# Kernel tuning notes

Hardware: AMD Instinct MI355X
Metric: run time of the kernel (lower is better)

The kernel has to match this reference:

```python
import jax, jax.numpy as jnp
import numpy as np

ST_HIDDEN = 128
ST_HEADS = 4
ST_LAYERS = 3
RES_SCALE = 1.0
DK = ST_HIDDEN // ST_HEADS


def build_3d_adj(spatial_ei, spatial_ea, n_nodes, window):
    # replicate spatial edges per time slice with node offset t*n_nodes
    offs = (jnp.arange(window) * n_nodes)[None, :, None]  # [1,W,1]
    all_sp_idx = (spatial_ei[:, None, :] + offs).reshape(2, -1)  # [2, W*E]
    all_sp_attr = jnp.tile(spatial_ea, (window, 1))  # [W*E, De]
    # temporal edges t -> t+1 for every node
    src = jnp.arange((window - 1) * n_nodes)
    temp_idx = jnp.stack([src, src + n_nodes], axis=0)  # [2, (W-1)*N]
    temp_attr = jnp.broadcast_to(spatial_ea.mean(axis=0, keepdims=True),
                                 (temp_idx.shape[1], spatial_ea.shape[1]))
    ei = jnp.concatenate([all_sp_idx, temp_idx], axis=1)
    ea = jnp.concatenate([all_sp_attr, temp_attr], axis=0)
    return ei, ea


def seg_softmax(logits, dst, num_nodes):
    # logits [E,H], segment softmax over dst (pyg_softmax)
    m = jax.ops.segment_max(logits, dst, num_segments=num_nodes)  # [N,H]
    ex = jnp.exp(logits - m[dst])
    s = jax.ops.segment_sum(ex, dst, num_segments=num_nodes)
    return ex / (s[dst] + 1e-16)


def layernorm(x, g, b, eps=1e-5):
    mu = x.mean(-1, keepdims=True)
    var = ((x - mu) ** 2).mean(-1, keepdims=True)
    return (x - mu) * jax.lax.rsqrt(var + eps) * g + b


def block(x, ei, ea, qw, qb, kw, kb, vw, vb, fw, fb, ow, ob, ln_g, ln_b):
    B, Nt, _ = x.shape
    H, dk = ST_HEADS, DK
    Q = (x @ qw + qb).reshape(B, Nt, H, dk)
    K = (x @ kw + kb).reshape(B, Nt, H, dk)
    V = (x @ vw + vb).reshape(B, Nt, H, dk)
    src, dst = ei[0], ei[1]
    q_e = Q[:, dst]  # [B,E,H,dk]
    k_e = K[:, src]
    v_e = V[:, src]
    film = ea @ fw + fb  # [E, 2*hidden]
    gamma, beta = jnp.split(film, 2, axis=-1)
    gamma = gamma.reshape(1, -1, H, dk)
    beta = beta.reshape(1, -1, H, dk)
    k_e = k_e * (1.0 + gamma) + beta
    logits = (q_e * k_e).sum(-1) / np.sqrt(dk).astype(np.float32)  # [B,E,H]
    att = jax.vmap(lambda l: seg_softmax(l, dst, Nt))(logits)
    msg = att[..., None] * v_e  # [B,E,H,dk]
    out = jnp.zeros((B, Nt, H, dk), x.dtype).at[:, dst].add(msg)
    y = out.reshape(B, Nt, H * dk) @ ow + ob
    return layernorm(x + y, ln_g, ln_b)


def setup_inputs() -> dict:
    key = jax.random.key(0)
    ks = jax.random.split(key, 12)
    B, W, N, Fin, E, De = 2, 16, 1000, 16, 16000, 8
    H, L = ST_HIDDEN, ST_LAYERS
    g = lambda k, s: jax.random.normal(k, s, jnp.float32) * 0.05
    return {
        "xw": jax.random.normal(ks[0], (B, W, N, Fin), jnp.float32),
        "spatial_ei": jax.random.randint(ks[1], (2, E), 0, N),
        "spatial_ea": jax.random.normal(ks[2], (E, De), jnp.float32),
        "in_w": g(ks[3], (Fin, H)), "in_b": jnp.zeros((H,), jnp.float32),
        "qw": g(ks[4], (L, H, H)), "qb": jnp.zeros((L, H), jnp.float32),
        "kw": g(ks[5], (L, H, H)), "kb": jnp.zeros((L, H), jnp.float32),
        "vw": g(ks[6], (L, H, H)), "vb": jnp.zeros((L, H), jnp.float32),
        "fw": g(ks[7], (L, De, 2 * H)), "fb": jnp.zeros((L, 2 * H), jnp.float32),
        "ow": g(ks[8], (L, H, H)), "ob": jnp.zeros((L, H), jnp.float32),
        "ln_g": jnp.ones((L, H), jnp.float32), "ln_b": jnp.zeros((L, H), jnp.float32),
        "head_w": g(ks[9], (H, 1)), "head_b": jnp.zeros((1,), jnp.float32),
    }


def reference(xw, spatial_ei, spatial_ea, in_w, in_b, qw, qb, kw, kb, vw, vb,
              fw, fb, ow, ob, ln_g, ln_b, head_w, head_b):
    B, W, N, Fin = xw.shape
    ei, ea = build_3d_adj(spatial_ei, spatial_ea, N, W)
    x = xw.reshape(B, W * N, Fin) @ in_w + in_b
    for l in range(ST_LAYERS):
        bx = block(x, ei, ea, qw[l], qb[l], kw[l], kb[l], vw[l], vb[l],
                   fw[l], fb[l], ow[l], ob[l], ln_g[l], ln_b[l])
        x = x + RES_SCALE * (bx - x)
    last = x.reshape(B, W, N, -1)[:, -1]  # [B,N,H]
    return jax.nn.softplus(last @ head_w + head_b).squeeze(-1)  # [B,N]
```

## Files before the change

kernel.cpp:

```cpp
#include <hip/hip_runtime.h>
#include <math.h>

constexpr int B    = 2;
constexpr int W    = 16;
constexpr int N    = 1000;
constexpr int FIN  = 16;
constexpr int E    = 16000;
constexpr int DE   = 8;
constexpr int H    = 128;
constexpr int L    = 3;
constexpr int WL   = 4;
constexpr int W0G  = 12;
constexpr int RPB  = WL * N;
constexpr int ROWS = B * RPB;
constexpr int NMAT = 12;

__device__ __forceinline__ float blockSum128(float v) {
  #pragma unroll
  for (int off = 32; off >= 1; off >>= 1) v += __shfl_xor(v, off);
  __shared__ float s2[2];
  int w = threadIdx.x >> 6;
  __syncthreads();
  if ((threadIdx.x & 63) == 0) s2[w] = v;
  __syncthreads();
  return s2[0] + s2[1];
}

__device__ __forceinline__ float dpp_add_xor1(float x) {
  int y = __builtin_amdgcn_update_dpp(0, __float_as_int(x), 0xB1, 0xF, 0xF, true);
  return x + __int_as_float(y);
}
__device__ __forceinline__ float dpp_add_xor2(float x) {
  int y = __builtin_amdgcn_update_dpp(0, __float_as_int(x), 0x4E, 0xF, 0xF, true);
  return x + __int_as_float(y);
}
__device__ __forceinline__ float headSum32(float p) {
  p = dpp_add_xor1(p);
  p = dpp_add_xor2(p);
  p += __shfl_xor(p, 4);
  p += __shfl_xor(p, 8);
  p += __shfl_xor(p, 16);
  return p;
}
__device__ __forceinline__ float dot4(float4 a, float4 b) {
  return a.x * b.x + a.y * b.y + a.z * b.z + a.w * b.w;
}

__global__ void k_count_scan(const int* __restrict__ ei, int* __restrict__ offs,
                             int* __restrict__ cursor, float* __restrict__ meanea) {
  __shared__ int cnt[N];
  __shared__ int scn[1024];
  int t = threadIdx.x;
  if (t < 8) meanea[t] = 0.f;
  if (t < N) cnt[t] = 0;
  __syncthreads();
  int vals[16];
  int nv = 0;
  for (int e = t; e < E; e += 1024) vals[nv++] = ei[E + e];
  for (int i = 0; i < nv; i++) atomicAdd(&cnt[vals[i]], 1);
  __syncthreads();
  int v = (t < N) ? cnt[t] : 0;
  scn[t] = v;
  __syncthreads();
  for (int st = 1; st < 1024; st <<= 1) {
    int add = (t >= st) ? scn[t - st] : 0;
    __syncthreads();
    scn[t] += add;
    __syncthreads();
  }
  if (t < N) {
    offs[t + 1] = scn[t];
    if (t == 0) offs[0] = 0;
    cursor[t] = scn[t] - v;
  }
}

__global__ void k_prep2(const int* __restrict__ ei, const float* __restrict__ ea,
                        int* __restrict__ cursor, int* __restrict__ csr_src,
                        int* __restrict__ csr_eid, float* __restrict__ meanea,
                        const float* __restrict__ qw, const float* __restrict__ kw,
                        const float* __restrict__ vw, const float* __restrict__ ow,
                        float4* __restrict__ wTp4,
                        const float* __restrict__ xw, const float* __restrict__ in_w,
                        const float* __restrict__ in_b, float* __restrict__ x) {
  int bid = blockIdx.x;
  int t = threadIdx.x;
  if (bid < 64) {
    int e = bid * 256 + t;
    if (e < E) {
      int src = ei[e];
      int dst = ei[E + e];
      int pos = atomicAdd(&cursor[dst], 1);
      csr_src[pos] = src;
      csr_eid[pos] = e;
    }
  } else if (bid < 128) {
    __shared__ float sbuf[256];
    int d = t & 7, g = t >> 3;
    float s = 0.f;
    for (int e = (bid - 64) * 32 + g; e < E; e += 64 * 32) s += ea[e * DE + d];
    sbuf[t] = s;
    __syncthreads();
    for (int st = 16; st >= 1; st >>= 1) {
      if (g < st) sbuf[g * 8 + d] += sbuf[(g + st) * 8 + d];
      __syncthreads();
    }
    if (g == 0) atomicAdd(&meanea[d], sbuf[d]);
  } else if (bid < 128 + NMAT * 16) {
    int bid2 = bid - 128;
    int mat = bid2 / 16;
    int pair = bid2 % 16;
    int kk4 = pair * 2 + (t >> 7);
    int c = t & 127;
    int l = mat >> 2, mm = mat & 3;
    const float* src = ((mm == 0) ? qw : (mm == 1) ? kw : (mm == 2) ? vw : ow) + (long)l * H * H;
    int k0 = kk4 * 4;
    float4 v4;
    v4.x = src[(k0 + 0) * H + c];
    v4.y = src[(k0 + 1) * H + c];
    v4.z = src[(k0 + 2) * H + c];
    v4.w = src[(k0 + 3) * H + c];
    wTp4[((long)mat * 32 + kk4) * H + c] = v4;
  } else {
    int bi = bid - (128 + NMAT * 16);
    int b = bi / 63, tt = bi % 63;
    int lr0 = tt * 64;
    __shared__ float xwS[64][FIN];
    __shared__ float inS[FIN][H];
    for (int i = t; i < 64 * FIN; i += 256) {
      int r = i >> 4, k = i & 15;
      int lr = lr0 + r;
      float val = 0.f;
      if (lr < RPB) {
        int wl = lr / N, n = lr % N;
        val = xw[(((long)b * W + (W0G + wl)) * N + n) * FIN + k];
      }
      xwS[r][k] = val;
    }
    for (int i = t; i < FIN * H; i += 256) inS[i >> 7][i & 127] = in_w[i];
    __syncthreads();
    #pragma unroll
    for (int qi = 0; qi < 8; qi++) {
      int idx = t + qi * 256;
      int r = idx >> 5, cq = idx & 31;
      int lr = lr0 + r;
      if (lr < RPB) {
        float4 acc = *(const float4*)(in_b + cq * 4);
        #pragma unroll
        for (int k = 0; k < FIN; k++) {
          float xv = xwS[r][k];
          float4 w4 = *(const float4*)(&inS[k][cq * 4]);
          acc.x += xv * w4.x; acc.y += xv * w4.y; acc.z += xv * w4.z; acc.w += xv * w4.w;
        }
        *(float4*)(x + ((long)b * RPB + lr) * H + cq * 4) = acc;
      }
    }
  }
}

__global__ void k_gemm(const float* __restrict__ X, const float4* __restrict__ wTp4,
                       int matBase,
                       const float* __restrict__ bq, const float* __restrict__ bk,
                       const float* __restrict__ bv,
                       float* __restrict__ Cq, float* __restrict__ Ck, float* __restrict__ Cv,
                       int base, int tiles) {
  int m = blockIdx.y;
  const float* bm = (m == 0) ? bq : (m == 1) ? bk : bv;
  float* Cm       = (m == 0) ? Cq : (m == 1) ? Ck : Cv;
  const float4* wp = wTp4 + (long)(matBase + m) * 32 * H;
  int bb = blockIdx.x / tiles;
  int tt = blockIdx.x % tiles;
  int lr0 = base + tt * 64;
  int t = threadIdx.x;
  int cg = t & 31, rg = t >> 5;
  __shared__ float xs[64][H];
  #pragma unroll
  for (int i = 0; i < 8; i++) {
    int row = i * 8 + rg;
    int lr = lr0 + row;
    float4 v4 = make_float4(0.f, 0.f, 0.f, 0.f);
    if (lr < RPB) v4 = *(const float4*)(X + ((long)bb * RPB + lr) * H + cg * 4);
    *(float4*)&xs[row][cg * 4] = v4;
  }
  __syncthreads();
  float4 bias4 = *(const float4*)(bm + cg * 4);
  float4 acc[8];
  #pragma unroll
  for (int i = 0; i < 8; i++) acc[i] = bias4;
  for (int kk4 = 0; kk4 < 32; kk4++) {
    float4 w0 = wp[kk4 * H + cg * 4 + 0];
    float4 w1 = wp[kk4 * H + cg * 4 + 1];
    float4 w2 = wp[kk4 * H + cg * 4 + 2];
    float4 w3 = wp[kk4 * H + cg * 4 + 3];
    #pragma unroll
    for (int i = 0; i < 8; i++) {
      float4 xv = *(const float4*)&xs[rg * 8 + i][kk4 * 4];
      acc[i].x += dot4(xv, w0);
      acc[i].y += dot4(xv, w1);
      acc[i].z += dot4(xv, w2);
      acc[i].w += dot4(xv, w3);
    }
  }
  #pragma unroll
  for (int i = 0; i < 8; i++) {
    int lr = lr0 + rg * 8 + i;
    if (lr < RPB) *(float4*)(Cm + ((long)bb * RPB + lr) * H + cg * 4) = acc[i];
  }
}

__global__ void k_attn_oln(const float* __restrict__ Qb, const float* __restrict__ Kb,
                           const float* __restrict__ Vb,
                           const float* __restrict__ ea, const float* __restrict__ meanea,
                           const float* __restrict__ fw, const float* __restrict__ fb,
                           const int* __restrict__ offs, const int* __restrict__ csr_src,
                           const int* __restrict__ csr_eid,
                           const float* __restrict__ x, const float4* __restrict__ owp,
                           const float* __restrict__ ob, const float* __restrict__ lng,
                           const float* __restrict__ lnb, float* __restrict__ xo,
                           int out_lo,
                           const float* __restrict__ hw, const float* __restrict__ hb,
                           float* __restrict__ out, int do_head) {
  int tid = threadIdx.x;
  float rgw[DE], rbw[DE];
  #pragma unroll
  for (int d = 0; d < DE; d++) {
    rgw[d] = fw[d * 2 * H + tid];
    rbw[d] = fw[d * 2 * H + H + tid];
  }
  int nwin = WL - out_lo;
  int idx = blockIdx.x;
  int b = idx / (nwin * N);
  int rem = idx % (nwin * N);
  int wl = out_lo + rem / N;
  int n = rem % N;
  long drow = ((long)b * WL + wl) * N + n;
  float q = Qb[drow * H + tid];
  float fbg = fb[tid], fbb = fb[H + tid];
  long sbase = ((long)b * WL + wl) * N;
  long trow  = ((long)b * WL + wl - 1) * N + n;
  const float scale = 0.17677669529663687f;
  int i0 = offs[n], i1 = offs[n + 1];

  float m = -INFINITY, ssum = 0.f, acc = 0.f;
  for (int base = i0; base <= i1; base += 4) {
    float l[4], vv[4];
    #pragma unroll
    for (int j = 0; j < 4; j++) {
      int i = base + j;
      if (i > i1) { l[j] = -INFINITY; vv[j] = 0.f; continue; }
      long srow; const float* eap; float esc;
      if (i < i1) { srow = sbase + csr_src[i]; eap = ea + (long)csr_eid[i] * DE; esc = 1.f; }
      else        { srow = trow;               eap = meanea;                    esc = 1.f / E; }
      float kv = Kb[srow * H + tid];
      vv[j]    = Vb[srow * H + tid];
      float4 a0 = *(const float4*)(eap);
      float4 a1 = *(const float4*)(eap + 4);
      float a[DE] = {a0.x * esc, a0.y * esc, a0.z * esc, a0.w * esc,
                     a1.x * esc, a1.y * esc, a1.z * esc, a1.w * esc};
      float g = fbg, be = fbb;
      #pragma unroll
      for (int d = 0; d < DE; d++) {
        g  += a[d] * rgw[d];
        be += a[d] * rbw[d];
      }
      float p = q * (kv * (1.f + g) + be);
      l[j] = headSum32(p) * scale;
    }
    float mn = m;
    #pragma unroll
    for (int j = 0; j < 4; j++) mn = fmaxf(mn, l[j]);
    float sc  = __expf(m - mn);
    float pe0 = __expf(l[0] - mn);
    float pe1 = __expf(l[1] - mn);
    float pe2 = __expf(l[2] - mn);
    float pe3 = __expf(l[3] - mn);
    ssum = ssum * sc + ((pe0 + pe1) + (pe2 + pe3));
    acc  = acc  * sc + ((pe0 * vv[0] + pe1 * vv[1]) + (pe2 * vv[2] + pe3 * vv[3]));
    m = mn;
  }
  float ab = acc / (ssum + 1e-16f);

  __shared__ float sab[H];
  sab[tid] = ab;
  __syncthreads();
  float y = ob[tid];
  #pragma unroll 4
  for (int kk4 = 0; kk4 < 32; kk4++) {
    float4 w4 = owp[kk4 * H + tid];
    float4 a4 = *(const float4*)&sab[kk4 * 4];
    y += dot4(a4, w4);
  }

  float v = x[drow * H + tid] + y;
  float mu = blockSum128(v) * (1.f / H);
  float dv = v - mu;
  float var = blockSum128(dv * dv) * (1.f / H);
  float o = dv * rsqrtf(var + 1e-5f) * lng[tid] + lnb[tid];

  if (!do_head) {
    xo[drow * H + tid] = o;
  } else {
    float hv = o * hw[tid];
    float tot = blockSum128(hv);
    if (tid == 0) {
      float z = tot + hb[0];
      out[b * N + n] = fmaxf(z, 0.f) + log1pf(expf(-fabsf(z)));
    }
  }
}

extern "C" void kernel_launch(void* const* d_in, const int* in_sizes, int n_in,
                              void* d_out, int out_size, void* d_ws, size_t ws_size,
                              hipStream_t stream) {
  const float* xw   = (const float*)d_in[0];
  const int*   ei   = (const int*)d_in[1];
  const float* ea   = (const float*)d_in[2];
  const float* in_w = (const float*)d_in[3];
  const float* in_b = (const float*)d_in[4];
  const float* qw   = (const float*)d_in[5];
  const float* qb   = (const float*)d_in[6];
  const float* kw   = (const float*)d_in[7];
  const float* kb   = (const float*)d_in[8];
  const float* vw   = (const float*)d_in[9];
  const float* vb   = (const float*)d_in[10];
  const float* fw   = (const float*)d_in[11];
  const float* fb   = (const float*)d_in[12];
  const float* ow   = (const float*)d_in[13];
  const float* ob   = (const float*)d_in[14];
  const float* ln_g = (const float*)d_in[15];
  const float* ln_b = (const float*)d_in[16];
  const float* hw   = (const float*)d_in[17];
  const float* hb   = (const float*)d_in[18];
  float* out = (float*)d_out;

  float* ws   = (float*)d_ws;
  float* x    = ws;
  float* x2   = x  + (long)ROWS * H;
  float* Qb   = x2 + (long)ROWS * H;
  float* Kb   = Qb + (long)ROWS * H;
  float* Vb   = Kb + (long)ROWS * H;
  float* wTp  = Vb + (long)ROWS * H;
  float* meanea = wTp + (long)NMAT * H * H;
  int* offs    = (int*)(meanea + 8);
  int* cursor  = offs + N + 1;
  int* csr_src = cursor + N;
  int* csr_eid = csr_src + E;
  float4* wTp4 = (float4*)wTp;

  k_count_scan<<<1, 1024, 0, stream>>>(ei, offs, cursor, meanea);
  k_prep2<<<128 + NMAT * 16 + 126, 256, 0, stream>>>(
      ei, ea, cursor, csr_src, csr_eid, meanea,
      qw, kw, vw, ow, wTp4, xw, in_w, in_b, x);

  float* xa = x;
  float* xb = x2;
  for (int l = 0; l < L; l++) {
    int in_lo = l, out_lo = l + 1;
    int rows_pb = (WL - in_lo) * N;
    int tiles = (rows_pb + 63) / 64;
    k_gemm<<<dim3(B * tiles, 3), 256, 0, stream>>>(
        xa, wTp4, l * 4, qb + (long)l * H, kb + (long)l * H, vb + (long)l * H,
        Qb, Kb, Vb, in_lo * N, tiles);
    int nout = B * (WL - out_lo) * N;
    int last = (l == L - 1) ? 1 : 0;
    k_attn_oln<<<nout, H, 0, stream>>>(
        Qb, Kb, Vb, ea, meanea,
        fw + (long)l * DE * 2 * H, fb + (long)l * 2 * H,
        offs, csr_src, csr_eid,
        xa, wTp4 + ((long)l * 4 + 3) * 32 * H, ob + (long)l * H,
        ln_g + (long)l * H, ln_b + (long)l * H, xb, out_lo,
        hw, hb, out, last);
    float* tmp = xa; xa = xb; xb = tmp;
  }
}
```

Before: 293.5 us.

## Precompute per-edge FiLM in bf16, drop online-max softmax, retile QKV gemm

Adds a per-layer kernel that computes FiLM gamma/beta for every edge once and stores them packed as bf16 pairs, so the attention kernel no longer redoes the 8-wide FiLM dot products for each destination and batch. The attention loop drops the running-max online softmax and accumulates plain exponentials, and src/eid are packed into one int2 CSR entry. The QKV gemm moves from a 64-row shared-memory tile to 2 rows per thread read directly from global memory, with more blocks. The bf16 FiLM values and the missing max-subtraction add rounding error and overflow risk, and the gemm loses shared-memory reuse of X.

```diff
diff --git a/kernel.cpp b/kernel.cpp
--- a/kernel.cpp
+++ b/kernel.cpp
@@ -76,8 +76,8 @@
 }
 
 __global__ void k_prep2(const int* __restrict__ ei, const float* __restrict__ ea,
-                        int* __restrict__ cursor, int* __restrict__ csr_src,
-                        int* __restrict__ csr_eid, float* __restrict__ meanea,
+                        int* __restrict__ cursor, int2* __restrict__ csr,
+                        float* __restrict__ meanea,
                         const float* __restrict__ qw, const float* __restrict__ kw,
                         const float* __restrict__ vw, const float* __restrict__ ow,
                         float4* __restrict__ wTp4,
@@ -91,8 +91,7 @@
       int src = ei[e];
       int dst = ei[E + e];
       int pos = atomicAdd(&cursor[dst], 1);
-      csr_src[pos] = src;
-      csr_eid[pos] = e;
+      csr[pos] = make_int2(src, e);
     }
   } else if (bid < 128) {
     __shared__ float sbuf[256];
@@ -158,6 +157,43 @@
   }
 }
 
+__global__ void k_film(const float* __restrict__ ea, const float* __restrict__ fw,
+                       const float* __restrict__ fb, const float* __restrict__ meanea,
+                       unsigned int* __restrict__ filmh) {
+  int e0 = blockIdx.x * 4;
+  int t = threadIdx.x;
+  float rgw[DE], rbw[DE];
+  #pragma unroll
+  for (int d = 0; d < DE; d++) {
+    rgw[d] = fw[d * 2 * H + t];
+    rbw[d] = fw[d * 2 * H + H + t];
+  }
+  float fbg = fb[t], fbb = fb[H + t];
+  for (int e = e0; e < e0 + 4 && e <= E; e++) {
+    float a[DE];
+    if (e < E) {
+      float4 a0 = *(const float4*)(ea + (long)e * DE);
+      float4 a1 = *(const float4*)(ea + (long)e * DE + 4);
+      a[0] = a0.x; a[1] = a0.y; a[2] = a0.z; a[3] = a0.w;
+      a[4] = a1.x; a[5] = a1.y; a[6] = a1.z; a[7] = a1.w;
+    } else {
+      #pragma unroll
+      for (int d = 0; d < DE; d++) a[d] = meanea[d] * (1.0f / E);
+    }
+    float g = fbg, be = fbb;
+    #pragma unroll
+    for (int d = 0; d < DE; d++) {
+      g  += a[d] * rgw[d];
+      be += a[d] * rbw[d];
+    }
+    unsigned int gb = __float_as_uint(g);
+    gb = (gb + 0x7fffu + ((gb >> 16) & 1u)) >> 16;
+    unsigned int bb_ = __float_as_uint(be);
+    bb_ = (bb_ + 0x7fffu + ((bb_ >> 16) & 1u)) & 0xffff0000u;
+    filmh[(long)e * H + t] = gb | bb_;
+  }
+}
+
 __global__ void k_gemm(const float* __restrict__ X, const float4* __restrict__ wTp4,
                        int matBase,
                        const float* __restrict__ bq, const float* __restrict__ bk,
@@ -170,50 +206,31 @@
   const float4* wp = wTp4 + (long)(matBase + m) * 32 * H;
   int bb = blockIdx.x / tiles;
   int tt = blockIdx.x % tiles;
-  int lr0 = base + tt * 64;
+  int lr0 = tt * 16;
   int t = threadIdx.x;
   int cg = t & 31, rg = t >> 5;
-  __shared__ float xs[64][H];
-  #pragma unroll
-  for (int i = 0; i < 8; i++) {
-    int row = i * 8 + rg;
-    int lr = lr0 + row;
-    float4 v4 = make_float4(0.f, 0.f, 0.f, 0.f);
-    if (lr < RPB) v4 = *(const float4*)(X + ((long)bb * RPB + lr) * H + cg * 4);
-    *(float4*)&xs[row][cg * 4] = v4;
-  }
-  __syncthreads();
+  long row0 = (long)bb * RPB + base + lr0 + rg * 2;
+  const float4* x0p = (const float4*)(X + row0 * H);
+  const float4* x1p = (const float4*)(X + (row0 + 1) * H);
   float4 bias4 = *(const float4*)(bm + cg * 4);
-  float4 acc[8];
-  #pragma unroll
-  for (int i = 0; i < 8; i++) acc[i] = bias4;
+  float4 acc0 = bias4, acc1 = bias4;
+  #pragma unroll 4
   for (int kk4 = 0; kk4 < 32; kk4++) {
-    float4 w0 = wp[kk4 * H + cg * 4 + 0];
-    float4 w1 = wp[kk4 * H + cg * 4 + 1];
-    float4 w2 = wp[kk4 * H + cg * 4 + 2];
-    float4 w3 = wp[kk4 * H + cg * 4 + 3];
-    #pragma unroll
-    for (int i = 0; i < 8; i++) {
-      float4 xv = *(const float4*)&xs[rg * 8 + i][kk4 * 4];
-      acc[i].x += dot4(xv, w0);
-      acc[i].y += dot4(xv, w1);
-      acc[i].z += dot4(xv, w2);
-      acc[i].w += dot4(xv, w3);
-    }
-  }
-  #pragma unroll
-  for (int i = 0; i < 8; i++) {
-    int lr = lr0 + rg * 8 + i;
-    if (lr < RPB) *(float4*)(Cm + ((long)bb * RPB + lr) * H + cg * 4) = acc[i];
-  }
+    float4 x0 = x0p[kk4];
+    float4 x1 = x1p[kk4];
+    const float4* wr = wp + kk4 * H + cg * 4;
+    float4 w0 = wr[0], w1 = wr[1], w2 = wr[2], w3 = wr[3];
+    acc0.x += dot4(x0, w0); acc0.y += dot4(x0, w1); acc0.z += dot4(x0, w2); acc0.w += dot4(x0, w3);
+    acc1.x += dot4(x1, w0); acc1.y += dot4(x1, w1); acc1.z += dot4(x1, w2); acc1.w += dot4(x1, w3);
+  }
+  *(float4*)(Cm + row0 * H + cg * 4) = acc0;
+  *(float4*)(Cm + (row0 + 1) * H + cg * 4) = acc1;
 }
 
 __global__ void k_attn_oln(const float* __restrict__ Qb, const float* __restrict__ Kb,
                            const float* __restrict__ Vb,
-                           const float* __restrict__ ea, const float* __restrict__ meanea,
-                           const float* __restrict__ fw, const float* __restrict__ fb,
-                           const int* __restrict__ offs, const int* __restrict__ csr_src,
-                           const int* __restrict__ csr_eid,
+                           const unsigned int* __restrict__ filmh,
+                           const int* __restrict__ offs, const int2* __restrict__ csr,
                            const float* __restrict__ x, const float4* __restrict__ owp,
                            const float* __restrict__ ob, const float* __restrict__ lng,
                            const float* __restrict__ lnb, float* __restrict__ xo,
@@ -221,12 +238,6 @@
                            const float* __restrict__ hw, const float* __restrict__ hb,
                            float* __restrict__ out, int do_head) {
   int tid = threadIdx.x;
-  float rgw[DE], rbw[DE];
-  #pragma unroll
-  for (int d = 0; d < DE; d++) {
-    rgw[d] = fw[d * 2 * H + tid];
-    rbw[d] = fw[d * 2 * H + H + tid];
-  }
   int nwin = WL - out_lo;
   int idx = blockIdx.x;
   int b = idx / (nwin * N);
@@ -235,48 +246,38 @@
   int n = rem % N;
   long drow = ((long)b * WL + wl) * N + n;
   float q = Qb[drow * H + tid];
-  float fbg = fb[tid], fbb = fb[H + tid];
   long sbase = ((long)b * WL + wl) * N;
   long trow  = ((long)b * WL + wl - 1) * N + n;
   const float scale = 0.17677669529663687f;
   int i0 = offs[n], i1 = offs[n + 1];
 
-  float m = -INFINITY, ssum = 0.f, acc = 0.f;
-  for (int base = i0; base <= i1; base += 4) {
-    float l[4], vv[4];
+  unsigned int fh = filmh[(long)E * H + tid];
+  float g  = __uint_as_float(fh << 16);
+  float be = __uint_as_float(fh & 0xffff0000u);
+  float kv = Kb[trow * H + tid];
+  float vv = Vb[trow * H + tid];
+  float p  = q * (kv * (1.f + g) + be);
+  float pe = __expf(headSum32(p) * scale);
+  float ssum = pe, acc = pe * vv;
+
+  for (int i4 = i0; i4 < i1; i4 += 4) {
     #pragma unroll
     for (int j = 0; j < 4; j++) {
-      int i = base + j;
-      if (i > i1) { l[j] = -INFINITY; vv[j] = 0.f; continue; }
-      long srow; const float* eap; float esc;
-      if (i < i1) { srow = sbase + csr_src[i]; eap = ea + (long)csr_eid[i] * DE; esc = 1.f; }
-      else        { srow = trow;               eap = meanea;                    esc = 1.f / E; }
-      float kv = Kb[srow * H + tid];
-      vv[j]    = Vb[srow * H + tid];
-      float4 a0 = *(const float4*)(eap);
-      float4 a1 = *(const float4*)(eap + 4);
-      float a[DE] = {a0.x * esc, a0.y * esc, a0.z * esc, a0.w * esc,
-                     a1.x * esc, a1.y * esc, a1.z * esc, a1.w * esc};
-      float g = fbg, be = fbb;
-      #pragma unroll
-      for (int d = 0; d < DE; d++) {
-        g  += a[d] * rgw[d];
-        be += a[d] * rbw[d];
-      }
-      float p = q * (kv * (1.f + g) + be);
-      l[j] = headSum32(p) * scale;
-    }
-    float mn = m;
-    #pragma unroll
-    for (int j = 0; j < 4; j++) mn = fmaxf(mn, l[j]);
-    float sc  = __expf(m - mn);
-    float pe0 = __expf(l[0] - mn);
-    float pe1 = __expf(l[1] - mn);
-    float pe2 = __expf(l[2] - mn);
-    float pe3 = __expf(l[3] - mn);
-    ssum = ssum * sc + ((pe0 + pe1) + (pe2 + pe3));
-    acc  = acc  * sc + ((pe0 * vv[0] + pe1 * vv[1]) + (pe2 * vv[2] + pe3 * vv[3]));
-    m = mn;
+      int i = i4 + j;
+      int ic = (i < i1) ? i : (i1 - 1);
+      int2 se = csr[ic];
+      long srow = sbase + se.x;
+      unsigned int f2 = filmh[(long)se.y * H + tid];
+      float g2 = __uint_as_float(f2 << 16);
+      float b2 = __uint_as_float(f2 & 0xffff0000u);
+      float kv2 = Kb[srow * H + tid];
+      float vv2 = Vb[srow * H + tid];
+      float p2  = q * (kv2 * (1.f + g2) + b2);
+      float pe2 = __expf(headSum32(p2) * scale);
+      pe2 = (i < i1) ? pe2 : 0.f;
+      ssum += pe2;
+      acc  += pe2 * vv2;
+    }
   }
   float ab = acc / (ssum + 1e-16f);
 
@@ -284,7 +285,7 @@
   sab[tid] = ab;
   __syncthreads();
   float y = ob[tid];
-  #pragma unroll 4
+  #pragma unroll 8
   for (int kk4 = 0; kk4 < 32; kk4++) {
     float4 w4 = owp[kk4 * H + tid];
     float4 a4 = *(const float4*)&sab[kk4 * 4];
@@ -340,33 +341,32 @@
   float* Kb   = Qb + (long)ROWS * H;
   float* Vb   = Kb + (long)ROWS * H;
   float* wTp  = Vb + (long)ROWS * H;
-  float* meanea = wTp + (long)NMAT * H * H;
+  unsigned int* filmh = (unsigned int*)(wTp + (long)NMAT * H * H);
+  float* meanea = (float*)(filmh + (long)(E + 1) * H);
   int* offs    = (int*)(meanea + 8);
   int* cursor  = offs + N + 1;
-  int* csr_src = cursor + N;
-  int* csr_eid = csr_src + E;
+  int2* csr    = (int2*)(cursor + N);
   float4* wTp4 = (float4*)wTp;
 
   k_count_scan<<<1, 1024, 0, stream>>>(ei, offs, cursor, meanea);
   k_prep2<<<128 + NMAT * 16 + 126, 256, 0, stream>>>(
-      ei, ea, cursor, csr_src, csr_eid, meanea,
-      qw, kw, vw, ow, wTp4, xw, in_w, in_b, x);
+      ei, ea, cursor, csr, meanea, qw, kw, vw, ow, wTp4, xw, in_w, in_b, x);
 
   float* xa = x;
   float* xb = x2;
   for (int l = 0; l < L; l++) {
     int in_lo = l, out_lo = l + 1;
+    k_film<<<(E + 1 + 3) / 4, 128, 0, stream>>>(
+        ea, fw + (long)l * DE * 2 * H, fb + (long)l * 2 * H, meanea, filmh);
     int rows_pb = (WL - in_lo) * N;
-    int tiles = (rows_pb + 63) / 64;
+    int tiles = rows_pb / 16;
     k_gemm<<<dim3(B * tiles, 3), 256, 0, stream>>>(
         xa, wTp4, l * 4, qb + (long)l * H, kb + (long)l * H, vb + (long)l * H,
         Qb, Kb, Vb, in_lo * N, tiles);
     int nout = B * (WL - out_lo) * N;
     int last = (l == L - 1) ? 1 : 0;
     k_attn_oln<<<nout, H, 0, stream>>>(
-        Qb, Kb, Vb, ea, meanea,
-        fw + (long)l * DE * 2 * H, fb + (long)l * 2 * H,
-        offs, csr_src, csr_eid,
+        Qb, Kb, Vb, filmh, offs, csr,
         xa, wTp4 + ((long)l * 4 + 3) * 32 * H, ob + (long)l * H,
         ln_g + (long)l * H, ln_b + (long)l * H, xb, out_lo,
         hw, hb, out, last);
```

New measurement: 326.0 us. 1.11x slower.
